# Kernel tuning notes

Measured on AMD Instinct MI355X. Metric: run time of the kernel, lower is better.

The kernel has to match this reference:

```python
import jax, jax.numpy as jnp
import numpy as np

B, M, D = 16, 16, 512          # m (tokens per sample) must equal num_experts
N = 16                          # num_experts
H = (D + D) * 2 // 3            # hidden_dim = 682
OUT = 512


def setup_inputs() -> dict:
    key = jax.random.key(0)
    ks = jax.random.split(key, 8)
    s = lambda k, shape, fan: jax.random.normal(k, shape, jnp.float32) / np.sqrt(fan)
    return {
        "x":    jax.random.normal(ks[0], (B, M, D), jnp.float32),
        "phi":  jax.random.normal(ks[1], (D, N, H), jnp.float32),
        "W1":   s(ks[2], (N, D, H), D),
        "b1":   s(ks[3], (N, H), D),
        "W2":   s(ks[4], (N, H, D), H),
        "b2":   s(ks[5], (N, D), H),
        "Wout": s(ks[6], (N * D, OUT), N * D),
        "bout": s(ks[7], (OUT,), N * D),
    }


def reference(x, phi, W1, b1, W2, b2, Wout, bout):
    # dispatch/combine logits: [b, m, n, p]
    logits = jnp.einsum('bmd,dnp->bmnp', x, phi)
    Dw = jax.nn.softmax(logits, axis=1)                       # dispatch weights over tokens m
    Cw = jax.nn.softmax(jax.nn.softmax(logits, axis=2), axis=3)  # (softmax of softmax, faithful)
    Xs = jnp.einsum('bmd,bmnp->bnpd', x, Dw)                  # expert slot inputs [b,n,p,d]
    # batched per-expert MLP (grouped GEMM over expert axis n)
    hmid = jax.nn.relu(jnp.einsum('bnpd,ndh->bnph', Xs, W1) + b1[None, :, None, :])
    Ys = jnp.einsum('bnph,nhd->bnpd', hmid, W2) + b2[None, :, None, :]
    Y = jnp.einsum('bnpd,bmnp->bmd', Ys, Cw)                  # combine -> [b, m, d]
    flat = Y.reshape(Y.shape[0], -1)                          # [b, m*d] == [b, n*d]
    return flat @ Wout + bout
```

## Files before the change

### kernel.cpp

```cpp
#include <hip/hip_runtime.h>
#include <hip/hip_bf16.h>
#include <math.h>

typedef unsigned int   u32;
typedef unsigned short u16;
typedef __bf16 bf16;
typedef bf16  bf16x8  __attribute__((ext_vector_type(8)));
typedef float f32x4   __attribute__((ext_vector_type(4)));
typedef float f32x16  __attribute__((ext_vector_type(16)));

#define BBATCH 16
#define MTOK   16
#define NEXP   16
#define DDIM   512
#define HDIM   682
#define HPAD   704
#define NHCOL  (NEXP*HDIM)
#define NHPCOL (NEXP*HPAD)
#define BM     (BBATCH*MTOK)

__device__ __forceinline__ u16 f2bf(float f) {
    u32 u = __builtin_bit_cast(u32, f);
    u += 0x7fffu + ((u >> 16) & 1u);
    return (u16)(u >> 16);
}
__device__ __forceinline__ float bf2f(u16 h) {
    u32 u = ((u32)h) << 16;
    return __builtin_bit_cast(float, u);
}
__device__ __forceinline__ u32 pk2bf(float a, float b) {
    __hip_bfloat162 t = __float22bfloat162_rn(float2{a, b});
    u32 r;
    __builtin_memcpy(&r, &t, 4);
    return r;
}

__global__ __launch_bounds__(256) void k_prep(
    const float* __restrict__ x, const float* __restrict__ b2,
    const float* __restrict__ bout,
    u16* __restrict__ xh, u16* __restrict__ xl,
    float* __restrict__ Y, float* __restrict__ out, u16* __restrict__ DwT) {
    const int bid = blockIdx.x, tid = threadIdx.x;
    if (bid < 128) {
        int i = (bid * 256 + tid) * 4;
        float4 v = *(const float4*)&x[i];
        float a[4] = {v.x, v.y, v.z, v.w};
        u16 hh[4], ll[4];
        #pragma unroll
        for (int j = 0; j < 4; ++j) {
            hh[j] = f2bf(a[j]);
            ll[j] = f2bf(a[j] - bf2f(hh[j]));
        }
        *(uint2*)&xh[i] = make_uint2((u32)hh[0] | ((u32)hh[1] << 16), (u32)hh[2] | ((u32)hh[3] << 16));
        *(uint2*)&xl[i] = make_uint2((u32)ll[0] | ((u32)ll[1] << 16), (u32)ll[2] | ((u32)ll[3] << 16));
    } else if (bid < 640) {
        int idx = (bid - 128) * 256 + tid;
        int d = idx & 511;
        float s = 0.f;
        #pragma unroll
        for (int nn = 0; nn < 16; ++nn) s += b2[nn * 512 + d];
        Y[idx] = s;
    } else if (bid < 672) {
        int idx = (bid - 640) * 256 + tid;
        out[idx] = bout[idx & 511];
    } else {
        int g = (bid - 672) * 256 + tid;
        int bn = g / 88, off = g - bn * 88;
        *(uint2*)(DwT + (size_t)(bn * HPAD + HDIM) * 16 + off * 4) = make_uint2(0u, 0u);
    }
}

__global__ __launch_bounds__(256) void k_lgemm(
    const u16* __restrict__ xh, const u16* __restrict__ xl,
    const float* __restrict__ phi, float* __restrict__ C,
    u16* __restrict__ DwT) {
    __shared__ u16 AH[128 * 40], AL[128 * 40], BH[64 * 40], BL[64 * 40];
    __shared__ float F[32 * 68];
    const int ct = blockIdx.x, rt = blockIdx.y;
    const int tid = threadIdx.x;
    const int wv = tid >> 6, lane = tid & 63, quad = lane >> 4, l15 = lane & 15;
    f32x4 acc[2][4] = {};
    for (int kb = 0; kb < 512; kb += 32) {
        {
            int rr = tid >> 2, kg = (tid & 3) * 8;
            #pragma unroll
            for (int rp = 0; rp < 2; ++rp) {
                int r = rp * 64 + rr;
                size_t ao = (size_t)(rt * 128 + r) * 512 + kb + kg;
                *(uint4*)&AH[r * 40 + kg] = *(const uint4*)(xh + ao);
                *(uint4*)&AL[r * 40 + kg] = *(const uint4*)(xl + ao);
            }
        }
        {
            int dl = tid >> 3, cg = (tid & 7) * 8;
            int c0 = ct * 64 + cg;
            const float* src = phi + (size_t)(kb + dl) * NHCOL + c0;
            float v[8];
            if (c0 + 8 <= NHCOL) {
                *(float4*)&v[0] = *(const float4*)&src[0];
                *(float4*)&v[4] = *(const float4*)&src[4];
            } else {
                #pragma unroll
                for (int i = 0; i < 8; ++i) v[i] = (c0 + i < NHCOL) ? src[i] : 0.f;
            }
            #pragma unroll
            for (int i = 0; i < 8; ++i) F[dl * 68 + cg + i] = v[i];
        }
        __syncthreads();
        {
            int cc = tid & 63, q = tid >> 6;
            u16 th[8], tl[8];
            #pragma unroll
            for (int i = 0; i < 8; ++i) {
                float v = F[(q * 8 + i) * 68 + cc];
                th[i] = f2bf(v);
                tl[i] = f2bf(v - bf2f(th[i]));
            }
            *(uint4*)&BH[cc * 40 + q * 8] = *(uint4*)&th[0];
            *(uint4*)&BL[cc * 40 + q * 8] = *(uint4*)&tl[0];
        }
        __syncthreads();
        bf16x8 ah[2], al[2];
        #pragma unroll
        for (int i = 0; i < 2; ++i) {
            ah[i] = *(const bf16x8*)&AH[(wv * 32 + i * 16 + l15) * 40 + quad * 8];
            al[i] = *(const bf16x8*)&AL[(wv * 32 + i * 16 + l15) * 40 + quad * 8];
        }
        #pragma unroll
        for (int j = 0; j < 4; ++j) {
            bf16x8 bh = *(const bf16x8*)&BH[(j * 16 + l15) * 40 + quad * 8];
            bf16x8 bl = *(const bf16x8*)&BL[(j * 16 + l15) * 40 + quad * 8];
            #pragma unroll
            for (int i = 0; i < 2; ++i) {
                acc[i][j] = __builtin_amdgcn_mfma_f32_16x16x32_bf16(ah[i], bh, acc[i][j], 0, 0, 0);
                acc[i][j] = __builtin_amdgcn_mfma_f32_16x16x32_bf16(ah[i], bl, acc[i][j], 0, 0, 0);
                acc[i][j] = __builtin_amdgcn_mfma_f32_16x16x32_bf16(al[i], bh, acc[i][j], 0, 0, 0);
            }
        }
        __syncthreads();
    }
    #pragma unroll
    for (int i = 0; i < 2; ++i) {
        const int b  = rt * 8 + wv * 2 + i;
        const int r0 = rt * 128 + wv * 32 + i * 16 + quad * 4;
        #pragma unroll
        for (int j = 0; j < 4; ++j) {
            const int col = ct * 64 + j * 16 + l15;
            float a0 = acc[i][j][0], a1 = acc[i][j][1], a2 = acc[i][j][2], a3 = acc[i][j][3];
            if (col < NHCOL) {
                C[(size_t)(r0 + 0) * NHCOL + col] = a0;
                C[(size_t)(r0 + 1) * NHCOL + col] = a1;
                C[(size_t)(r0 + 2) * NHCOL + col] = a2;
                C[(size_t)(r0 + 3) * NHCOL + col] = a3;
            }
            float mx = fmaxf(fmaxf(a0, a1), fmaxf(a2, a3));
            mx = fmaxf(mx, __shfl_xor(mx, 16));
            mx = fmaxf(mx, __shfl_xor(mx, 32));
            float e0 = expf(a0 - mx), e1 = expf(a1 - mx);
            float e2 = expf(a2 - mx), e3 = expf(a3 - mx);
            float s = e0 + e1 + e2 + e3;
            s += __shfl_xor(s, 16);
            s += __shfl_xor(s, 32);
            float inv = 1.f / s;
            if (col < NHCOL) {
                int n = col / HDIM;
                int p = col - n * HDIM;
                u16* dst = DwT + ((size_t)((b * 16 + n) * HPAD + p)) * 16 + quad * 4;
                *(uint2*)dst = make_uint2(pk2bf(e0 * inv, e1 * inv), pk2bf(e2 * inv, e3 * inv));
            }
        }
    }
}

__global__ __launch_bounds__(256) void k_t1cw(
    const u16* __restrict__ A, const float* __restrict__ W1,
    u16* __restrict__ T1b,
    const float* __restrict__ L, u16* __restrict__ CwB) {
    __shared__ __align__(16) char smem[NHCOL * 4];
    const int bid = blockIdx.x, tid = threadIdx.x;
    if (bid < 176) {
        u16*   As = (u16*)smem;
        u16*   Bs = (u16*)(smem + 20480);
        float* F  = (float*)(smem + 25600);
        const int ct = bid;
        const int wv = tid >> 6, lane = tid & 63, quad = lane >> 4, l15 = lane & 15;
        const int n = ct / 11, h0 = (ct % 11) * 64;
        f32x4 acc[4][4] = {};
        for (int kb = 0; kb < 512; kb += 32) {
            {
                int rr = tid >> 2, kg = (tid & 3) * 8;
                #pragma unroll
                for (int rp = 0; rp < 4; ++rp) {
                    int r = rp * 64 + rr;
                    *(uint4*)&As[r * 40 + kg] = *(const uint4*)(A + (size_t)r * 512 + kb + kg);
                }
            }
            {
                int dl = tid >> 3, cg = (tid & 7) * 8;
                int h = h0 + cg;
                const float* wr = W1 + ((size_t)n * 512 + kb + dl) * HDIM + h;
                float v[8];
                if (h + 8 <= HDIM) {
                    #pragma unroll
                    for (int i = 0; i < 4; ++i) {
                        float2 t = *(const float2*)&wr[i * 2];
                        v[i * 2] = t.x; v[i * 2 + 1] = t.y;
                    }
                } else {
                    #pragma unroll
                    for (int i = 0; i < 8; ++i) v[i] = (h + i < HDIM) ? wr[i] : 0.f;
                }
                #pragma unroll
                for (int i = 0; i < 8; ++i) F[dl * 68 + cg + i] = v[i];
            }
            __syncthreads();
            {
                int cc = tid & 63, q = tid >> 6;
                u16 tv[8];
                #pragma unroll
                for (int i = 0; i < 8; ++i) tv[i] = f2bf(F[(q * 8 + i) * 68 + cc]);
                *(uint4*)&Bs[cc * 40 + q * 8] = *(uint4*)&tv[0];
            }
            __syncthreads();
            bf16x8 af[4], bfr[4];
            #pragma unroll
            for (int i = 0; i < 4; ++i)
                af[i] = *(const bf16x8*)&As[(wv * 64 + i * 16 + l15) * 40 + quad * 8];
            #pragma unroll
            for (int j = 0; j < 4; ++j)
                bfr[j] = *(const bf16x8*)&Bs[(j * 16 + l15) * 40 + quad * 8];
            #pragma unroll
            for (int i = 0; i < 4; ++i)
                #pragma unroll
                for (int j = 0; j < 4; ++j)
                    acc[i][j] = __builtin_amdgcn_mfma_f32_16x16x32_bf16(af[i], bfr[j], acc[i][j], 0, 0, 0);
            __syncthreads();
        }
        #pragma unroll
        for (int i = 0; i < 4; ++i)
            #pragma unroll
            for (int j = 0; j < 4; ++j) {
                int col = ct * 64 + j * 16 + l15;
                int r0  = wv * 64 + i * 16 + quad * 4;
                #pragma unroll
                for (int r = 0; r < 4; ++r)
                    T1b[(size_t)(r0 + r) * NHPCOL + col] = f2bf(acc[i][j][r]);
            }
    } else {
        float* row = (float*)smem;
        const int j = bid - 176;
        const int m = j & 15, b = j >> 4;
        const float* Lrow = L + (size_t)(b * 16 + m) * NHCOL;
        for (int i = tid; i < NHCOL; i += 256) row[i] = Lrow[i];
        __syncthreads();
        for (int p = tid; p < HDIM; p += 256) {
            float v[16];
            float mx = -1e30f;
            #pragma unroll
            for (int n = 0; n < 16; ++n) { v[n] = row[n * HDIM + p]; mx = fmaxf(mx, v[n]); }
            float s = 0.f;
            #pragma unroll
            for (int n = 0; n < 16; ++n) { v[n] = expf(v[n] - mx); s += v[n]; }
            float inv = 1.f / s;
            #pragma unroll
            for (int n = 0; n < 16; ++n) row[n * HDIM + p] = expf(v[n] * inv);
        }
        __syncthreads();
        const int wv = tid >> 6, lane = tid & 63;
        for (int nn = 0; nn < 4; ++nn) {
            int n = wv * 4 + nn;
            float s = 0.f;
            for (int p = lane; p < HDIM; p += 64) s += row[n * HDIM + p];
            #pragma unroll
            for (int off = 32; off > 0; off >>= 1) s += __shfl_xor(s, off);
            float inv = 1.f / s;
            u16* dst = CwB + (size_t)(((b * 16 + n) * 16 + m)) * HPAD;
            for (int p = lane; p < HDIM; p += 64) dst[p] = f2bf(row[n * HDIM + p] * inv);
            if (lane < HPAD - HDIM) dst[HDIM + lane] = 0;
        }
    }
}

__global__ __launch_bounds__(256) void k_mid(
    const u16* __restrict__ T1b, const u16* __restrict__ DwT,
    const u16* __restrict__ CwB, const float* __restrict__ b1,
    u16* __restrict__ Gb) {
    __shared__ u16 T1T[128 * 24];
    __shared__ u16 hmidT[128 * 64];
    const int ht = blockIdx.x, n = blockIdx.y, b = blockIdx.z;
    const int tid = threadIdx.x;
    const int wv = tid >> 6, lane = tid & 63;
    const int quad = lane >> 4, l15 = lane & 15;
    const int l31 = lane & 31, half = lane >> 5;
    const int h0 = ht * 128;
    const int b16n = b * 16 + n;

    {
        int m = tid & 15, hh0 = (tid >> 4) * 8;
        u16 v[8];
        if (h0 + hh0 + 8 <= HPAD) {
            *(uint4*)v = *(const uint4*)(T1b + (size_t)(b * 16 + m) * NHPCOL + n * HPAD + h0 + hh0);
        } else {
            #pragma unroll
            for (int i = 0; i < 8; ++i) v[i] = 0;
        }
        #pragma unroll
        for (int i = 0; i < 8; ++i) T1T[(hh0 + i) * 24 + m] = v[i];
    }
    __syncthreads();

    const int hrow = wv * 32 + l31;
    bf16x8 bt1 = *(const bf16x8*)&T1T[hrow * 24 + half * 8];
    int hg1 = h0 + hrow;
    float biasf = (hg1 < HDIM) ? b1[n * HDIM + hg1] : 0.f;
    f32x16 cbias;
    #pragma unroll
    for (int i = 0; i < 16; ++i) cbias[i] = biasf;

    const u16* dwbase = DwT + (size_t)(b16n * HPAD) * 16;
    const u16* cwrow  = CwB + (size_t)(b16n * 16 + l15) * HPAD;

    f32x4 acc[2] = {};
    const int hsw = hrow & 7;
    for (int c = 0; c < 11; ++c) {
        const int p0 = c * 64;
        #pragma unroll
        for (int pt = 0; pt < 2; ++pt) {
            bf16x8 adw = *(const bf16x8*)(dwbase + (size_t)(p0 + pt * 32 + l31) * 16 + half * 8);
            f32x16 hm = __builtin_amdgcn_mfma_f32_32x32x16_bf16(adw, bt1, cbias, 0, 0, 0);
            #pragma unroll
            for (int g = 0; g < 4; ++g) {
                float v0 = fmaxf(hm[g * 4 + 0], 0.f);
                float v1 = fmaxf(hm[g * 4 + 1], 0.f);
                float v2 = fmaxf(hm[g * 4 + 2], 0.f);
                float v3 = fmaxf(hm[g * 4 + 3], 0.f);
                uint2 pk = make_uint2(pk2bf(v0, v1), pk2bf(v2, v3));
                int gran = (pt * 4 + g) ^ hsw;
                *(uint2*)&hmidT[hrow * 64 + gran * 8 + half * 4] = pk;
            }
        }
        #pragma unroll
        for (int s = 0; s < 2; ++s) {
            bf16x8 acw = *(const bf16x8*)(cwrow + p0 + s * 32 + quad * 8);
            #pragma unroll
            for (int hj = 0; hj < 2; ++hj) {
                int hr = wv * 32 + hj * 16 + l15;
                int gr = (s * 4 + quad) ^ (hr & 7);
                bf16x8 bh = *(const bf16x8*)&hmidT[hr * 64 + gr * 8];
                acc[hj] = __builtin_amdgcn_mfma_f32_16x16x32_bf16(acw, bh, acc[hj], 0, 0, 0);
            }
        }
    }
    #pragma unroll
    for (int hj = 0; hj < 2; ++hj) {
        int h = h0 + wv * 32 + hj * 16 + l15;
        if (h < HPAD) {
            #pragma unroll
            for (int r = 0; r < 4; ++r) {
                int m = quad * 4 + r;
                Gb[(size_t)(b * 16 + m) * NHPCOL + n * HPAD + h] = f2bf(acc[hj][r]);
            }
        }
    }
}

__global__ __launch_bounds__(256) void k_ygemm(
    const u16* __restrict__ G, const float* __restrict__ W2, float* __restrict__ Y) {
    __shared__ u16 AsL[64 * 40];
    __shared__ u16 BsL[128 * 40];
    __shared__ float F[32 * 132];
    const int ct = blockIdx.x, rt = blockIdx.y, nz = blockIdx.z;
    const int n = nz >> 1, kb0 = (nz & 1) * 352;
    const int tid = threadIdx.x;
    const int wv = tid >> 6, lane = tid & 63, quad = lane >> 4, l15 = lane & 15;
    const int m0 = rt * 64, d0 = ct * 128;
    f32x4 acc[4][2] = {};
    for (int kb = kb0; kb < kb0 + 352; kb += 32) {
        {
            int am = tid >> 2, akg = (tid & 3) * 8;
            *(uint4*)&AsL[am * 40 + akg] =
                *(const uint4*)(G + (size_t)(m0 + am) * NHPCOL + n * HPAD + kb + akg);
        }
        {
            int hl = tid >> 3, cg = (tid & 7) * 16;
            int h = kb + hl;
            float v[16];
            if (h < HDIM) {
                const float* src = W2 + ((size_t)n * HDIM + h) * 512 + d0 + cg;
                *(float4*)&v[0]  = *(const float4*)&src[0];
                *(float4*)&v[4]  = *(const float4*)&src[4];
                *(float4*)&v[8]  = *(const float4*)&src[8];
                *(float4*)&v[12] = *(const float4*)&src[12];
            } else {
                #pragma unroll
                for (int i = 0; i < 16; ++i) v[i] = 0.f;
            }
            #pragma unroll
            for (int i = 0; i < 16; ++i) F[hl * 132 + cg + i] = v[i];
        }
        __syncthreads();
        {
            int cc = tid & 127, half = tid >> 7;
            u16 tv[16];
            #pragma unroll
            for (int i = 0; i < 16; ++i) tv[i] = f2bf(F[(half * 16 + i) * 132 + cc]);
            *(uint4*)&BsL[cc * 40 + half * 16]     = *(uint4*)&tv[0];
            *(uint4*)&BsL[cc * 40 + half * 16 + 8] = *(uint4*)&tv[8];
        }
        __syncthreads();
        bf16x8 af[4], bfr[2];
        #pragma unroll
        for (int i = 0; i < 4; ++i) af[i] = *(const bf16x8*)&AsL[(i * 16 + l15) * 40 + quad * 8];
        #pragma unroll
        for (int j = 0; j < 2; ++j) bfr[j] = *(const bf16x8*)&BsL[(wv * 32 + j * 16 + l15) * 40 + quad * 8];
        #pragma unroll
        for (int i = 0; i < 4; ++i)
            #pragma unroll
            for (int j = 0; j < 2; ++j)
                acc[i][j] = __builtin_amdgcn_mfma_f32_16x16x32_bf16(af[i], bfr[j], acc[i][j], 0, 0, 0);
        __syncthreads();
    }
    #pragma unroll
    for (int i = 0; i < 4; ++i)
        #pragma unroll
        for (int j = 0; j < 2; ++j) {
            int d = d0 + wv * 32 + j * 16 + l15;
            int r0 = m0 + i * 16 + quad * 4;
            #pragma unroll
            for (int r = 0; r < 4; ++r)
                atomicAdd(&Y[(size_t)(r0 + r) * 512 + d], acc[i][j][r]);
        }
}

__global__ __launch_bounds__(256) void k_outgemm(
    const float* __restrict__ Y, const float* __restrict__ Wout, float* __restrict__ out) {
    __shared__ u16 AsL[16 * 40];
    __shared__ u16 BsL[128 * 40];
    __shared__ float F[32 * 132];
    const int ct = blockIdx.x, ks = blockIdx.y;
    const int tid = threadIdx.x;
    const int wv = tid >> 6, lane = tid & 63, quad = lane >> 4, l15 = lane & 15;
    const int o0 = ct * 128, kbase = ks * 128;
    f32x4 acc[2] = {};
    for (int kb = 0; kb < 128; kb += 32) {
        {
            int r = tid >> 4, k2 = (tid & 15) * 2;
            float2 v = *(const float2*)&Y[(size_t)r * 8192 + kbase + kb + k2];
            AsL[r * 40 + k2]     = f2bf(v.x);
            AsL[r * 40 + k2 + 1] = f2bf(v.y);
        }
        {
            int kl = tid >> 3, cg = (tid & 7) * 16;
            const float* src = Wout + (size_t)(kbase + kb + kl) * 512 + o0 + cg;
            float v[16];
            *(float4*)&v[0]  = *(const float4*)&src[0];
            *(float4*)&v[4]  = *(const float4*)&src[4];
            *(float4*)&v[8]  = *(const float4*)&src[8];
            *(float4*)&v[12] = *(const float4*)&src[12];
            #pragma unroll
            for (int i = 0; i < 16; ++i) F[kl * 132 + cg + i] = v[i];
        }
        __syncthreads();
        {
            int cc = tid & 127, half = tid >> 7;
            u16 tv[16];
            #pragma unroll
            for (int i = 0; i < 16; ++i) tv[i] = f2bf(F[(half * 16 + i) * 132 + cc]);
            *(uint4*)&BsL[cc * 40 + half * 16]     = *(uint4*)&tv[0];
            *(uint4*)&BsL[cc * 40 + half * 16 + 8] = *(uint4*)&tv[8];
        }
        __syncthreads();
        bf16x8 af = *(const bf16x8*)&AsL[l15 * 40 + quad * 8];
        #pragma unroll
        for (int j = 0; j < 2; ++j) {
            bf16x8 bfr = *(const bf16x8*)&BsL[(wv * 32 + j * 16 + l15) * 40 + quad * 8];
            acc[j] = __builtin_amdgcn_mfma_f32_16x16x32_bf16(af, bfr, acc[j], 0, 0, 0);
        }
        __syncthreads();
    }
    #pragma unroll
    for (int j = 0; j < 2; ++j) {
        int o = o0 + wv * 32 + j * 16 + l15;
        #pragma unroll
        for (int r = 0; r < 4; ++r)
            atomicAdd(&out[(size_t)(quad * 4 + r) * 512 + o], acc[j][r]);
    }
}

extern "C" void kernel_launch(void* const* d_in, const int* in_sizes, int n_in,
                              void* d_out, int out_size, void* d_ws, size_t ws_size,
                              hipStream_t stream) {
    const float* x    = (const float*)d_in[0];
    const float* phi  = (const float*)d_in[1];
    const float* W1   = (const float*)d_in[2];
    const float* b1   = (const float*)d_in[3];
    const float* W2   = (const float*)d_in[4];
    const float* b2   = (const float*)d_in[5];
    const float* Wout = (const float*)d_in[6];
    const float* bout = (const float*)d_in[7];
    float* out = (float*)d_out;

    char* base = (char*)d_ws;
    float* logits = (float*)(base + 0);
    u16*   DwT    = (u16*)(base + 11173888);
    u16*   CwB    = (u16*)(base + 16941056);
    u16*   T1b    = (u16*)(base + 22708224);
    u16*   Gb     = (u16*)(base + 28475392);
    u16*   xh     = (u16*)(base + 34242560);
    u16*   xl     = (u16*)(base + 34504704);
    float* Y      = (float*)(base + 34766848);

    k_prep    <<<dim3(760), 256, 0, stream>>>(x, b2, bout, xh, xl, Y, out, DwT);
    k_lgemm   <<<dim3(171, 2), 256, 0, stream>>>(xh, xl, phi, logits, DwT);
    k_t1cw    <<<dim3(432), 256, 0, stream>>>(xh, W1, T1b, logits, CwB);
    k_mid     <<<dim3(6, 16, 16), 256, 0, stream>>>(T1b, DwT, CwB, b1, Gb);
    k_ygemm   <<<dim3(4, 4, 32), 256, 0, stream>>>(Gb, W2, Y);
    k_outgemm <<<dim3(4, 64), 256, 0, stream>>>(Y, Wout, out);
}
```

Measured before the change: 233.9 us.

## Co-schedule logits GEMM with T1 GEMM and split tiles for more blocks

The logits GEMM (x·phi, split-bf16) and the independent x·W1 GEMM now run in one launch, with a block-index branch choosing which one each block does. Both use smaller row tiles (64 rows for logits, 128 rows for T1), which produces many more blocks to fill the GPU's compute units. The Cw double-softmax moves to its own kernel because it depends on the finished logits. The output GEMM's K-split is also halved in depth to double its block count. The cost is more reloading of phi and W1 tiles and more atomic or partial-sum traffic, in exchange for better occupancy and overlap.

```diff
diff --git a/kernel.cpp b/kernel.cpp
--- a/kernel.cpp
+++ b/kernel.cpp
@@ -17,7 +17,6 @@
 #define HPAD   704
 #define NHCOL  (NEXP*HDIM)
 #define NHPCOL (NEXP*HPAD)
-#define BM     (BBATCH*MTOK)
 
 __device__ __forceinline__ u16 f2bf(float f) {
     u32 u = __builtin_bit_cast(u32, f);
@@ -70,88 +69,80 @@
     }
 }
 
-__global__ __launch_bounds__(256) void k_lgemm(
+__global__ __launch_bounds__(256) void k_lt1(
     const u16* __restrict__ xh, const u16* __restrict__ xl,
-    const float* __restrict__ phi, float* __restrict__ C,
-    u16* __restrict__ DwT) {
-    __shared__ u16 AH[128 * 40], AL[128 * 40], BH[64 * 40], BL[64 * 40];
-    __shared__ float F[32 * 68];
-    const int ct = blockIdx.x, rt = blockIdx.y;
-    const int tid = threadIdx.x;
+    const float* __restrict__ phi, const float* __restrict__ W1,
+    float* __restrict__ logits, u16* __restrict__ DwT, u16* __restrict__ T1b) {
+    __shared__ __align__(16) char SMEM[29184];
+    const int bid = blockIdx.x, tid = threadIdx.x;
     const int wv = tid >> 6, lane = tid & 63, quad = lane >> 4, l15 = lane & 15;
-    f32x4 acc[2][4] = {};
-    for (int kb = 0; kb < 512; kb += 32) {
-        {
-            int rr = tid >> 2, kg = (tid & 3) * 8;
-            #pragma unroll
-            for (int rp = 0; rp < 2; ++rp) {
-                int r = rp * 64 + rr;
-                size_t ao = (size_t)(rt * 128 + r) * 512 + kb + kg;
+    if (bid < 684) {
+        const int ct = bid % 171, rt = bid / 171;
+        u16* AH = (u16*)SMEM;
+        u16* AL = (u16*)(SMEM + 5120);
+        u16* BH = (u16*)(SMEM + 10240);
+        u16* BL = (u16*)(SMEM + 15360);
+        float* F = (float*)(SMEM + 20480);
+        f32x4 acc[4] = {};
+        for (int kb = 0; kb < 512; kb += 32) {
+            {
+                int r = tid >> 2, kg = (tid & 3) * 8;
+                size_t ao = (size_t)(rt * 64 + r) * 512 + kb + kg;
                 *(uint4*)&AH[r * 40 + kg] = *(const uint4*)(xh + ao);
                 *(uint4*)&AL[r * 40 + kg] = *(const uint4*)(xl + ao);
             }
-        }
-        {
-            int dl = tid >> 3, cg = (tid & 7) * 8;
-            int c0 = ct * 64 + cg;
-            const float* src = phi + (size_t)(kb + dl) * NHCOL + c0;
-            float v[8];
-            if (c0 + 8 <= NHCOL) {
-                *(float4*)&v[0] = *(const float4*)&src[0];
-                *(float4*)&v[4] = *(const float4*)&src[4];
-            } else {
-                #pragma unroll
-                for (int i = 0; i < 8; ++i) v[i] = (c0 + i < NHCOL) ? src[i] : 0.f;
-            }
-            #pragma unroll
-            for (int i = 0; i < 8; ++i) F[dl * 68 + cg + i] = v[i];
-        }
-        __syncthreads();
-        {
-            int cc = tid & 63, q = tid >> 6;
-            u16 th[8], tl[8];
-            #pragma unroll
-            for (int i = 0; i < 8; ++i) {
-                float v = F[(q * 8 + i) * 68 + cc];
-                th[i] = f2bf(v);
-                tl[i] = f2bf(v - bf2f(th[i]));
-            }
-            *(uint4*)&BH[cc * 40 + q * 8] = *(uint4*)&th[0];
-            *(uint4*)&BL[cc * 40 + q * 8] = *(uint4*)&tl[0];
-        }
-        __syncthreads();
-        bf16x8 ah[2], al[2];
-        #pragma unroll
-        for (int i = 0; i < 2; ++i) {
-            ah[i] = *(const bf16x8*)&AH[(wv * 32 + i * 16 + l15) * 40 + quad * 8];
-            al[i] = *(const bf16x8*)&AL[(wv * 32 + i * 16 + l15) * 40 + quad * 8];
-        }
-        #pragma unroll
-        for (int j = 0; j < 4; ++j) {
-            bf16x8 bh = *(const bf16x8*)&BH[(j * 16 + l15) * 40 + quad * 8];
-            bf16x8 bl = *(const bf16x8*)&BL[(j * 16 + l15) * 40 + quad * 8];
-            #pragma unroll
-            for (int i = 0; i < 2; ++i) {
-                acc[i][j] = __builtin_amdgcn_mfma_f32_16x16x32_bf16(ah[i], bh, acc[i][j], 0, 0, 0);
-                acc[i][j] = __builtin_amdgcn_mfma_f32_16x16x32_bf16(ah[i], bl, acc[i][j], 0, 0, 0);
-                acc[i][j] = __builtin_amdgcn_mfma_f32_16x16x32_bf16(al[i], bh, acc[i][j], 0, 0, 0);
-            }
-        }
-        __syncthreads();
-    }
-    #pragma unroll
-    for (int i = 0; i < 2; ++i) {
-        const int b  = rt * 8 + wv * 2 + i;
-        const int r0 = rt * 128 + wv * 32 + i * 16 + quad * 4;
+            {
+                int dl = tid >> 3, cg = (tid & 7) * 8;
+                int c0 = ct * 64 + cg;
+                const float* src = phi + (size_t)(kb + dl) * NHCOL + c0;
+                float v[8];
+                if (c0 + 8 <= NHCOL) {
+                    *(float4*)&v[0] = *(const float4*)&src[0];
+                    *(float4*)&v[4] = *(const float4*)&src[4];
+                } else {
+                    #pragma unroll
+                    for (int i = 0; i < 8; ++i) v[i] = (c0 + i < NHCOL) ? src[i] : 0.f;
+                }
+                #pragma unroll
+                for (int i = 0; i < 8; ++i) F[dl * 68 + cg + i] = v[i];
+            }
+            __syncthreads();
+            {
+                int cc = tid & 63, q = tid >> 6;
+                u16 th[8], tl[8];
+                #pragma unroll
+                for (int i = 0; i < 8; ++i) {
+                    float v = F[(q * 8 + i) * 68 + cc];
+                    th[i] = f2bf(v);
+                    tl[i] = f2bf(v - bf2f(th[i]));
+                }
+                *(uint4*)&BH[cc * 40 + q * 8] = *(uint4*)&th[0];
+                *(uint4*)&BL[cc * 40 + q * 8] = *(uint4*)&tl[0];
+            }
+            __syncthreads();
+            bf16x8 ah = *(const bf16x8*)&AH[(wv * 16 + l15) * 40 + quad * 8];
+            bf16x8 al = *(const bf16x8*)&AL[(wv * 16 + l15) * 40 + quad * 8];
+            #pragma unroll
+            for (int j = 0; j < 4; ++j) {
+                bf16x8 bh = *(const bf16x8*)&BH[(j * 16 + l15) * 40 + quad * 8];
+                bf16x8 bl = *(const bf16x8*)&BL[(j * 16 + l15) * 40 + quad * 8];
+                acc[j] = __builtin_amdgcn_mfma_f32_16x16x32_bf16(ah, bh, acc[j], 0, 0, 0);
+                acc[j] = __builtin_amdgcn_mfma_f32_16x16x32_bf16(ah, bl, acc[j], 0, 0, 0);
+                acc[j] = __builtin_amdgcn_mfma_f32_16x16x32_bf16(al, bh, acc[j], 0, 0, 0);
+            }
+            __syncthreads();
+        }
+        const int b  = rt * 4 + wv;
+        const int r0 = rt * 64 + wv * 16 + quad * 4;
         #pragma unroll
         for (int j = 0; j < 4; ++j) {
             const int col = ct * 64 + j * 16 + l15;
-            float a0 = acc[i][j][0], a1 = acc[i][j][1], a2 = acc[i][j][2], a3 = acc[i][j][3];
+            float a0 = acc[j][0], a1 = acc[j][1], a2 = acc[j][2], a3 = acc[j][3];
             if (col < NHCOL) {
-                C[(size_t)(r0 + 0) * NHCOL + col] = a0;
-                C[(size_t)(r0 + 1) * NHCOL + col] = a1;
-                C[(size_t)(r0 + 2) * NHCOL + col] = a2;
-                C[(size_t)(r0 + 3) * NHCOL + col] = a3;
+                logits[(size_t)(r0 + 0) * NHCOL + col] = a0;
+                logits[(size_t)(r0 + 1) * NHCOL + col] = a1;
+                logits[(size_t)(r0 + 2) * NHCOL + col] = a2;
+                logits[(size_t)(r0 + 3) * NHCOL + col] = a3;
             }
             float mx = fmaxf(fmaxf(a0, a1), fmaxf(a2, a3));
             mx = fmaxf(mx, __shfl_xor(mx, 16));
@@ -169,31 +160,20 @@
                 *(uint2*)dst = make_uint2(pk2bf(e0 * inv, e1 * inv), pk2bf(e2 * inv, e3 * inv));
             }
         }
-    }
-}
-
-__global__ __launch_bounds__(256) void k_t1cw(
-    const u16* __restrict__ A, const float* __restrict__ W1,
-    u16* __restrict__ T1b,
-    const float* __restrict__ L, u16* __restrict__ CwB) {
-    __shared__ __align__(16) char smem[NHCOL * 4];
-    const int bid = blockIdx.x, tid = threadIdx.x;
-    if (bid < 176) {
-        u16*   As = (u16*)smem;
-        u16*   Bs = (u16*)(smem + 20480);
-        float* F  = (float*)(smem + 25600);
-        const int ct = bid;
-        const int wv = tid >> 6, lane = tid & 63, quad = lane >> 4, l15 = lane & 15;
+    } else {
+        const int w = bid - 684;
+        const int ct = w >> 1, rh = w & 1;
         const int n = ct / 11, h0 = (ct % 11) * 64;
-        f32x4 acc[4][4] = {};
+        u16* As = (u16*)SMEM;
+        u16* Bs = (u16*)(SMEM + 10240);
+        float* F = (float*)(SMEM + 15360);
+        f32x4 acc[2][4] = {};
         for (int kb = 0; kb < 512; kb += 32) {
             {
-                int rr = tid >> 2, kg = (tid & 3) * 8;
-                #pragma unroll
-                for (int rp = 0; rp < 4; ++rp) {
-                    int r = rp * 64 + rr;
-                    *(uint4*)&As[r * 40 + kg] = *(const uint4*)(A + (size_t)r * 512 + kb + kg);
-                }
+                int r = tid >> 1, kg = (tid & 1) * 16;
+                const u16* s = xh + (size_t)(rh * 128 + r) * 512 + kb + kg;
+                *(uint4*)&As[r * 40 + kg]     = *(const uint4*)s;
+                *(uint4*)&As[r * 40 + kg + 8] = *(const uint4*)(s + 8);
             }
             {
                 int dl = tid >> 3, cg = (tid & 7) * 8;
@@ -222,62 +202,65 @@
                 *(uint4*)&Bs[cc * 40 + q * 8] = *(uint4*)&tv[0];
             }
             __syncthreads();
-            bf16x8 af[4], bfr[4];
-            #pragma unroll
-            for (int i = 0; i < 4; ++i)
-                af[i] = *(const bf16x8*)&As[(wv * 64 + i * 16 + l15) * 40 + quad * 8];
+            bf16x8 af[2], bfr[4];
+            #pragma unroll
+            for (int i = 0; i < 2; ++i)
+                af[i] = *(const bf16x8*)&As[(wv * 32 + i * 16 + l15) * 40 + quad * 8];
             #pragma unroll
             for (int j = 0; j < 4; ++j)
                 bfr[j] = *(const bf16x8*)&Bs[(j * 16 + l15) * 40 + quad * 8];
             #pragma unroll
-            for (int i = 0; i < 4; ++i)
+            for (int i = 0; i < 2; ++i)
                 #pragma unroll
                 for (int j = 0; j < 4; ++j)
                     acc[i][j] = __builtin_amdgcn_mfma_f32_16x16x32_bf16(af[i], bfr[j], acc[i][j], 0, 0, 0);
             __syncthreads();
         }
         #pragma unroll
-        for (int i = 0; i < 4; ++i)
+        for (int i = 0; i < 2; ++i)
             #pragma unroll
             for (int j = 0; j < 4; ++j) {
                 int col = ct * 64 + j * 16 + l15;
-                int r0  = wv * 64 + i * 16 + quad * 4;
+                int r0  = rh * 128 + wv * 32 + i * 16 + quad * 4;
                 #pragma unroll
                 for (int r = 0; r < 4; ++r)
                     T1b[(size_t)(r0 + r) * NHPCOL + col] = f2bf(acc[i][j][r]);
             }
-    } else {
-        float* row = (float*)smem;
-        const int j = bid - 176;
-        const int m = j & 15, b = j >> 4;
-        const float* Lrow = L + (size_t)(b * 16 + m) * NHCOL;
-        for (int i = tid; i < NHCOL; i += 256) row[i] = Lrow[i];
-        __syncthreads();
-        for (int p = tid; p < HDIM; p += 256) {
-            float v[16];
-            float mx = -1e30f;
-            #pragma unroll
-            for (int n = 0; n < 16; ++n) { v[n] = row[n * HDIM + p]; mx = fmaxf(mx, v[n]); }
-            float s = 0.f;
-            #pragma unroll
-            for (int n = 0; n < 16; ++n) { v[n] = expf(v[n] - mx); s += v[n]; }
-            float inv = 1.f / s;
-            #pragma unroll
-            for (int n = 0; n < 16; ++n) row[n * HDIM + p] = expf(v[n] * inv);
-        }
-        __syncthreads();
-        const int wv = tid >> 6, lane = tid & 63;
-        for (int nn = 0; nn < 4; ++nn) {
-            int n = wv * 4 + nn;
-            float s = 0.f;
-            for (int p = lane; p < HDIM; p += 64) s += row[n * HDIM + p];
-            #pragma unroll
-            for (int off = 32; off > 0; off >>= 1) s += __shfl_xor(s, off);
-            float inv = 1.f / s;
-            u16* dst = CwB + (size_t)(((b * 16 + n) * 16 + m)) * HPAD;
-            for (int p = lane; p < HDIM; p += 64) dst[p] = f2bf(row[n * HDIM + p] * inv);
-            if (lane < HPAD - HDIM) dst[HDIM + lane] = 0;
-        }
+    }
+}
+
+__global__ __launch_bounds__(256) void k_cw(
+    const float* __restrict__ L, u16* __restrict__ CwB) {
+    __shared__ float row[NHCOL];
+    const int bid = blockIdx.x, tid = threadIdx.x;
+    const int m = bid & 15, b = bid >> 4;
+    const float* Lrow = L + (size_t)(b * 16 + m) * NHCOL;
+    for (int i = tid; i < NHCOL; i += 256) row[i] = Lrow[i];
+    __syncthreads();
+    for (int p = tid; p < HDIM; p += 256) {
+        float v[16];
+        float mx = -1e30f;
+        #pragma unroll
+        for (int n = 0; n < 16; ++n) { v[n] = row[n * HDIM + p]; mx = fmaxf(mx, v[n]); }
+        float s = 0.f;
+        #pragma unroll
+        for (int n = 0; n < 16; ++n) { v[n] = expf(v[n] - mx); s += v[n]; }
+        float inv = 1.f / s;
+        #pragma unroll
+        for (int n = 0; n < 16; ++n) row[n * HDIM + p] = expf(v[n] * inv);
+    }
+    __syncthreads();
+    const int wv = tid >> 6, lane = tid & 63;
+    for (int nn = 0; nn < 4; ++nn) {
+        int n = wv * 4 + nn;
+        float s = 0.f;
+        for (int p = lane; p < HDIM; p += 64) s += row[n * HDIM + p];
+        #pragma unroll
+        for (int off = 32; off > 0; off >>= 1) s += __shfl_xor(s, off);
+        float inv = 1.f / s;
+        u16* dst = CwB + (size_t)(((b * 16 + n) * 16 + m)) * HPAD;
+        for (int p = lane; p < HDIM; p += 64) dst[p] = f2bf(row[n * HDIM + p] * inv);
+        if (lane < HPAD - HDIM) dst[HDIM + lane] = 0;
     }
 }
 
@@ -440,9 +423,9 @@
     const int ct = blockIdx.x, ks = blockIdx.y;
     const int tid = threadIdx.x;
     const int wv = tid >> 6, lane = tid & 63, quad = lane >> 4, l15 = lane & 15;
-    const int o0 = ct * 128, kbase = ks * 128;
+    const int o0 = ct * 128, kbase = ks * 64;
     f32x4 acc[2] = {};
-    for (int kb = 0; kb < 128; kb += 32) {
+    for (int kb = 0; kb < 64; kb += 32) {
         {
             int r = tid >> 4, k2 = (tid & 15) * 2;
             float2 v = *(const float2*)&Y[(size_t)r * 8192 + kbase + kb + k2];
@@ -511,9 +494,9 @@
     float* Y      = (float*)(base + 34766848);
 
     k_prep    <<<dim3(760), 256, 0, stream>>>(x, b2, bout, xh, xl, Y, out, DwT);
-    k_lgemm   <<<dim3(171, 2), 256, 0, stream>>>(xh, xl, phi, logits, DwT);
-    k_t1cw    <<<dim3(432), 256, 0, stream>>>(xh, W1, T1b, logits, CwB);
+    k_lt1     <<<dim3(1036), 256, 0, stream>>>(xh, xl, phi, W1, logits, DwT, T1b);
+    k_cw      <<<dim3(256), 256, 0, stream>>>(logits, CwB);
     k_mid     <<<dim3(6, 16, 16), 256, 0, stream>>>(T1b, DwT, CwB, b1, Gb);
     k_ygemm   <<<dim3(4, 4, 32), 256, 0, stream>>>(Gb, W2, Y);
-    k_outgemm <<<dim3(4, 64), 256, 0, stream>>>(Y, Wout, out);
-}
+    k_outgemm <<<dim3(4, 128), 256, 0, stream>>>(Y, Wout, out);
+}
```

New measurement: 226.0 us. 3.4% less time.
